# Optimization experiments

Hardware: AMD Instinct MI355X
Metric: run time of the kernel (lower is better)

Reference implementation:

```python
import jax, jax.numpy as jnp
import numpy as np

B, C, H, W = 32, 256, 32, 32   # batch, channels (inplanes==planes), spatial
E = 8                          # num_experts
EPS = 1e-5                     # BatchNorm eps


def setup_inputs() -> dict:
    key = jax.random.key(0)
    ks = jax.random.split(key, 6)
    s = 0.05
    return {
        "x": jax.random.normal(ks[0], (B, C, H, W), dtype=jnp.float32),
        # router: GAP -> Linear(C, E) -> sigmoid
        "router_w": jax.random.normal(ks[1], (E, C), dtype=jnp.float32) * s,
        "router_b": jnp.zeros((E,), dtype=jnp.float32),
        # expert kernel banks for the two CondConv2d layers (OIHW per expert)
        "w1": jax.random.normal(ks[2], (E, C, C, 3, 3), dtype=jnp.float32) * s,
        "w2": jax.random.normal(ks[3], (E, C, C, 3, 3), dtype=jnp.float32) * s,
        # BatchNorm (eval mode: running stats) params for bn1/bn2
        "g1": jnp.ones((C,), jnp.float32), "b1": jnp.zeros((C,), jnp.float32),
        "m1": jnp.zeros((C,), jnp.float32), "v1": jnp.ones((C,), jnp.float32),
        "g2": jnp.ones((C,), jnp.float32), "b2": jnp.zeros((C,), jnp.float32),
        "m2": jnp.zeros((C,), jnp.float32), "v2": jnp.ones((C,), jnp.float32),
    }


def _bn(x, g, b, m, v):
    # eval-mode BatchNorm over channel dim 1
    scale = (g * jax.lax.rsqrt(v + EPS))[None, :, None, None]
    shift = (b - m * g * jax.lax.rsqrt(v + EPS))[None, :, None, None]
    return x * scale + shift


def _cond_conv(x, w_bank, r):
    # x: [B,C,H,W]; w_bank: [E,O,I,3,3]; r: [B,E]
    # combine expert kernels per sample, then per-sample 3x3 conv (pad=1, stride=1)
    k = jnp.einsum('be,eoihw->boihw', r, w_bank)  # [B,O,I,3,3]

    def one(xb, kb):
        return jax.lax.conv_general_dilated(
            xb[None], kb, window_strides=(1, 1), padding=[(1, 1), (1, 1)],
            dimension_numbers=('NCHW', 'OIHW', 'NCHW'))[0]

    return jax.vmap(one)(x, k)  # [B,O,H,W]


def reference(x, router_w, router_b, w1, w2, g1, b1, m1, v1, g2, b2, m2, v2):
    # BasicRouter: global average pool -> linear -> sigmoid
    r = jax.nn.sigmoid(jnp.mean(x, axis=(2, 3)) @ router_w.T + router_b)  # [B,E]
    # drop_expert is identity in eval mode (training=False)
    out = jax.nn.relu(_bn(_cond_conv(x, w1, r), g1, b1, m1, v1))
    out = _bn(_cond_conv(out, w2, r), g2, b2, m2, v2)
    return jax.nn.relu(out + x)  # identity residual (stride=1, inplanes==planes)
```

## Files before the change

### kernel.cpp

```cpp
#include <hip/hip_runtime.h>

typedef unsigned short ushort_t;
typedef __attribute__((ext_vector_type(8))) __bf16 bf16x8;
typedef __attribute__((ext_vector_type(4))) float f32x4;
typedef __attribute__((ext_vector_type(4))) int i32x4;
typedef __attribute__((ext_vector_type(4))) unsigned short u16x4;

#define BN_EPS 1e-5f
#define EPAD 136

#define BAR()    __builtin_amdgcn_s_barrier()
#define VMCNT4() asm volatile("s_waitcnt vmcnt(4)" ::: "memory")
#define VMCNT0() asm volatile("s_waitcnt vmcnt(0)" ::: "memory")
#define LGKM0()  asm volatile("s_waitcnt lgkmcnt(0)" ::: "memory")

__device__ __forceinline__ ushort_t f2bf(float f) {
    union { float f; unsigned u; } v; v.f = f;
    unsigned r = v.u + 0x7FFFu + ((v.u >> 16) & 1u);
    return (ushort_t)(r >> 16);
}
__device__ __forceinline__ float bf2f(ushort_t h) {
    union { unsigned u; float f; } v; v.u = ((unsigned)h) << 16; return v.f;
}

__device__ __forceinline__ void async_cp16(const ushort_t* g, ushort_t* l) {
    __builtin_amdgcn_global_load_lds(
        (const __attribute__((address_space(1))) unsigned int*)g,
        (__attribute__((address_space(3))) unsigned int*)l, 16, 0, 0);
}

__global__ void transpose_gap_kernel(const float* __restrict__ x, ushort_t* __restrict__ xt,
                                     float* __restrict__ gapsum) {
    __shared__ float tile[32][33];
    int b = blockIdx.z, c0 = blockIdx.y * 32, p0 = blockIdx.x * 32;
    int tx = threadIdx.x & 31, ty = threadIdx.x >> 5;
    float ps[4];
    #pragma unroll
    for (int i = 0; i < 4; ++i) {
        int c = ty + i * 8;
        float v = x[((long)b * 256 + c0 + c) * 1024 + p0 + tx];
        tile[c][tx] = v;
        ps[i] = v;
    }
    #pragma unroll
    for (int off = 16; off; off >>= 1)
        #pragma unroll
        for (int i = 0; i < 4; ++i) ps[i] += __shfl_down(ps[i], off, 32);
    if (tx == 0)
        #pragma unroll
        for (int i = 0; i < 4; ++i) atomicAdd(&gapsum[b * 256 + c0 + ty + i * 8], ps[i]);
    __syncthreads();
    #pragma unroll
    for (int i = 0; i < 4; ++i) {
        int p = ty + i * 8;
        xt[((long)b * 1024 + p0 + p) * 256 + c0 + tx] = f2bf(tile[tx][p]);
    }
}

__global__ void router_linear_kernel(const float* __restrict__ gapsum, const float* __restrict__ rw,
                                     const float* __restrict__ rb, float* __restrict__ r) {
    int t = threadIdx.x, b = t >> 3, e = t & 7;
    float s = 0.f;
    for (int c = 0; c < 256; ++c) s += gapsum[b * 256 + c] * rw[e * 256 + c];
    r[t] = 1.f / (1.f + expf(-(s * (1.f / 1024.f) + rb[e])));
}

__global__ __launch_bounds__(256, 4) void combine_kernel(const float* __restrict__ w,
                                                         const float* __restrict__ r,
                                                         ushort_t* __restrict__ ko) {
    __shared__ float wl[9216];
    const int t = threadIdx.x;
    const int g0 = blockIdx.x * 128;
    const int b0 = blockIdx.y * 8;

    #pragma unroll
    for (int it = 0; it < 9; ++it) {
        int lin = it * 256 + t;
        int e = lin / 288, rem = lin - e * 288;
        f32x4 v = *(const f32x4*)(w + (long)e * 589824 + (long)g0 * 9 + rem * 4);
        *(f32x4*)(&wl[lin * 4]) = v;
    }
    __syncthreads();

    const int g = t & 127;
    const int half = t >> 7;
    float wv[8][9];
    #pragma unroll
    for (int e = 0; e < 8; ++e)
        #pragma unroll
        for (int p = 0; p < 9; ++p)
            wv[e][p] = wl[e * 1152 + g * 9 + p];

    #pragma unroll
    for (int j = 0; j < 4; ++j) {
        int b = b0 + half * 4 + j;
        float rv[8];
        #pragma unroll
        for (int e = 0; e < 8; ++e) rv[e] = r[b * 8 + e];
        #pragma unroll
        for (int p = 0; p < 9; ++p) {
            float s = 0.f;
            #pragma unroll
            for (int e = 0; e < 8; ++e) s += rv[e] * wv[e][p];
            ko[((long)(b * 9 + p)) * 65536 + g0 + g] = f2bf(s);
        }
    }
}

template <int MODE>
__global__ __launch_bounds__(256, 2) void gemm_conv(
    const ushort_t* __restrict__ xin,
    const ushort_t* __restrict__ kbank,
    void* __restrict__ outp,
    const float* __restrict__ gam, const float* __restrict__ bet,
    const float* __restrict__ mu, const float* __restrict__ var,
    const ushort_t* __restrict__ residt) {
    __shared__ ushort_t smem[29440];
    ushort_t* ldsB = smem;
    ushort_t* ldsA = smem + 13056;

    const int t = threadIdx.x;
    const int lane = t & 63;
    const int lane15 = lane & 15;
    const int quad = lane >> 4;
    const int wv = t >> 6;
    const int id = blockIdx.x;
    const int q  = id >> 3;
    const int mt = q & 1;
    const int nt = (q >> 1) & 7;
    const int b  = (id & 7) + ((q >> 4) << 3);
    const int h0 = nt * 4;
    const int p0 = nt * 128;
    const int mw0 = (wv >> 1) * 64;
    const int nw0 = (wv & 1) * 64;
    const int wbase = t & ~63;

    f32x4 acc[4][4];
    #pragma unroll
    for (int i = 0; i < 4; ++i)
        #pragma unroll
        for (int j = 0; j < 4; ++j) acc[i][j] = 0.f;

    if (t < 96) {
        int rix = t >> 3, j = t & 7;
        int pi = (rix >> 1) * 34 + (rix & 1) * 33;
        i32x4 z = 0;
        *(i32x4*)(&ldsB[(pi * 8 + j) * 8]) = z;
    }
    if (nt == 0) { i32x4 z = 0; *(i32x4*)(&ldsB[(8 + t) * 8]) = z; }
    if (nt == 7) { i32x4 z = 0; *(i32x4*)(&ldsB[((5 * 34 + 1) * 8 + t) * 8]) = z; }

    const long xbase = (long)b * 1024 * 256;
    const long kbase = (long)b * 9 * 65536;

    auto stageB = [&](int kc) {
        #pragma unroll
        for (int hh = 0; hh < 6; ++hh) {
            int hg = h0 + hh - 1;
            if (hg < 0 || hg >= 32) continue;
            int ww = t >> 3;
            int pi = hh * 34 + 1 + ww;
            int jd = (t & 7) ^ (pi & 7);
            async_cp16(xin + xbase + (long)(hg * 32 + ww) * 256 + kc * 64 + jd * 8,
                       ldsB + ((hh * 34 + 1) * 8 + wbase) * 8);
        }
    };
    auto stageA = [&](int kc, int pos, int buf) {
        const ushort_t* srcA = kbank + kbase + (long)pos * 65536 + (long)mt * 32768 + kc * 64;
        ushort_t* base = ldsA + buf * 8192;
        #pragma unroll
        for (int it = 0; it < 4; ++it) {
            int s = it * 256 + t;
            int row = s >> 3;
            int k8 = (s & 7) ^ (row & 7);
            async_cp16(srcA + (long)row * 256 + k8 * 8, base + (it * 256 + wbase) * 8);
        }
    };

    stageB(0);
    stageA(0, 0, 0);
    __syncthreads();

    int par = 0;
    for (int kc = 0; kc < 4; ++kc) {
        for (int pos = 0; pos < 9; ++pos) {
            const bool last = (kc == 3 && pos == 8);
            if (!last) {
                int nk = kc, np = pos + 1;
                if (np == 9) { np = 0; ++nk; }
                stageA(nk, np, par ^ 1);
                VMCNT4();
            } else {
                VMCNT0();
            }
            BAR();

            const int dh = pos / 3 - 1, dw = pos % 3 - 1;
            const ushort_t* ab = ldsA + par * 8192;
            bf16x8 af[2][4], bv[2][4];
            #pragma unroll
            for (int kb = 0; kb < 2; ++kb) {
                int jk = kb * 4 + quad;
                #pragma unroll
                for (int mf = 0; mf < 4; ++mf) {
                    int row = mw0 + mf * 16 + lane15;
                    af[kb][mf] = *(const bf16x8*)(ab + (row * 8 + (jk ^ (row & 7))) * 8);
                }
                #pragma unroll
                for (int nf = 0; nf < 4; ++nf) {
                    int n = nw0 + nf * 16 + lane15;
                    int pi = ((n >> 5) + 1 + dh) * 34 + (n & 31) + 1 + dw;
                    bv[kb][nf] = *(const bf16x8*)(&ldsB[(pi * 8 + (jk ^ (pi & 7))) * 8]);
                }
            }
            LGKM0();
            BAR();

            if (pos == 8 && kc < 3) stageB(kc + 1);

            __builtin_amdgcn_s_setprio(1);
            #pragma unroll
            for (int kb = 0; kb < 2; ++kb)
                #pragma unroll
                for (int mf = 0; mf < 4; ++mf)
                    #pragma unroll
                    for (int nf = 0; nf < 4; ++nf)
                        acc[mf][nf] = __builtin_amdgcn_mfma_f32_16x16x32_bf16(af[kb][mf], bv[kb][nf], acc[mf][nf], 0, 0, 0);
            __builtin_amdgcn_s_setprio(0);
            par ^= 1;
        }
    }

    u16x4 rres[4][4];
    if (MODE == 1) {
        #pragma unroll
        for (int mf = 0; mf < 4; ++mf)
            #pragma unroll
            for (int nf = 0; nf < 4; ++nf) {
                int p = p0 + nw0 + nf * 16 + lane15;
                int cb = mt * 128 + mw0 + mf * 16 + quad * 4;
                rres[mf][nf] = *(const u16x4*)(residt + ((long)b * 1024 + p) * 256 + cb);
            }
    }

    float sc[4][4], sh[4][4];
    #pragma unroll
    for (int mf = 0; mf < 4; ++mf)
        #pragma unroll
        for (int i = 0; i < 4; ++i) {
            int c = mt * 128 + mw0 + mf * 16 + quad * 4 + i;
            float s = gam[c] * rsqrtf(var[c] + BN_EPS);
            sc[mf][i] = s;
            sh[mf][i] = bet[c] - mu[c] * s;
        }

    if (MODE == 0) {
        __syncthreads();
        ushort_t* ldsE = smem;
        #pragma unroll
        for (int mf = 0; mf < 4; ++mf)
            #pragma unroll
            for (int nf = 0; nf < 4; ++nf) {
                int pl = nw0 + nf * 16 + lane15;
                int cb = mw0 + mf * 16 + quad * 4;
                u16x4 pk;
                #pragma unroll
                for (int i = 0; i < 4; ++i) {
                    float v = acc[mf][nf][i] * sc[mf][i] + sh[mf][i];
                    pk[i] = f2bf(fmaxf(v, 0.f));
                }
                *(u16x4*)(&ldsE[pl * EPAD + cb]) = pk;
            }
        __syncthreads();
        ushort_t* op = (ushort_t*)outp;
        #pragma unroll
        for (int it = 0; it < 8; ++it) {
            int s = t + it * 256;
            int row = s >> 4, l16 = s & 15;
            i32x4 v = *(i32x4*)(&ldsE[row * EPAD + l16 * 8]);
            *(i32x4*)(op + ((long)b * 1024 + p0 + row) * 256 + mt * 128 + l16 * 8) = v;
        }
    } else {
        float* op = (float*)outp;
        #pragma unroll
        for (int mf = 0; mf < 4; ++mf)
            #pragma unroll
            for (int nf = 0; nf < 4; ++nf) {
                int p = p0 + nw0 + nf * 16 + lane15;
                #pragma unroll
                for (int i = 0; i < 4; ++i) {
                    int c = mt * 128 + mw0 + mf * 16 + quad * 4 + i;
                    float v = acc[mf][nf][i] * sc[mf][i] + sh[mf][i] + bf2f(rres[mf][nf][i]);
                    op[((long)b * 256 + c) * 1024 + p] = fmaxf(v, 0.f);
                }
            }
    }
}

extern "C" void kernel_launch(void* const* d_in, const int* in_sizes, int n_in,
                              void* d_out, int out_size, void* d_ws, size_t ws_size,
                              hipStream_t stream) {
    const float* x  = (const float*)d_in[0];
    const float* rw = (const float*)d_in[1];
    const float* rb = (const float*)d_in[2];
    const float* w1 = (const float*)d_in[3];
    const float* w2 = (const float*)d_in[4];
    const float* g1 = (const float*)d_in[5];
    const float* b1 = (const float*)d_in[6];
    const float* m1 = (const float*)d_in[7];
    const float* v1 = (const float*)d_in[8];
    const float* g2 = (const float*)d_in[9];
    const float* b2 = (const float*)d_in[10];
    const float* m2 = (const float*)d_in[11];
    const float* v2 = (const float*)d_in[12];

    const size_t GAP_OFF = 4096;
    const size_t XT_OFF  = 36864;
    const size_t O1_OFF  = XT_OFF + (size_t)16777216;
    const size_t KB_OFF  = O1_OFF + (size_t)16777216;
    const size_t NEED    = KB_OFF + (size_t)32 * 9 * 65536 * 2;
    if (ws_size < NEED) return;

    char* ws = (char*)d_ws;
    float* r       = (float*)ws;
    float* gapsum  = (float*)(ws + GAP_OFF);
    ushort_t* xt   = (ushort_t*)(ws + XT_OFF);
    ushort_t* o1   = (ushort_t*)(ws + O1_OFF);
    ushort_t* kbuf = (ushort_t*)(ws + KB_OFF);

    hipMemsetAsync(gapsum, 0, 32768, stream);
    transpose_gap_kernel<<<dim3(32, 8, 32), 256, 0, stream>>>(x, xt, gapsum);
    router_linear_kernel<<<1, 256, 0, stream>>>(gapsum, rw, rb, r);
    combine_kernel<<<dim3(512, 4), 256, 0, stream>>>(w1, r, kbuf);
    gemm_conv<0><<<512, 256, 0, stream>>>(xt, kbuf, (void*)o1, g1, b1, m1, v1, nullptr);
    combine_kernel<<<dim3(512, 4), 256, 0, stream>>>(w2, r, kbuf);
    gemm_conv<1><<<512, 256, 0, stream>>>(o1, kbuf, d_out, g2, b2, m2, v2, xt);
}
```

Measured before the change: 255.0 us.

## Load conv weight tiles straight to registers, drop LDS staging and per-iteration barriers

```diff
diff --git a/kernel.cpp b/kernel.cpp
--- a/kernel.cpp
+++ b/kernel.cpp
@@ -10,7 +10,7 @@
 #define EPAD 136
 
 #define BAR()    __builtin_amdgcn_s_barrier()
-#define VMCNT4() asm volatile("s_waitcnt vmcnt(4)" ::: "memory")
+#define VMCNT8() asm volatile("s_waitcnt vmcnt(8)" ::: "memory")
 #define VMCNT0() asm volatile("s_waitcnt vmcnt(0)" ::: "memory")
 #define LGKM0()  asm volatile("s_waitcnt lgkmcnt(0)" ::: "memory")
 
@@ -115,9 +115,9 @@
     const float* __restrict__ gam, const float* __restrict__ bet,
     const float* __restrict__ mu, const float* __restrict__ var,
     const ushort_t* __restrict__ residt) {
-    __shared__ ushort_t smem[29440];
+    constexpr int SMEMN = (MODE == 0) ? 17408 : 13056;
+    __shared__ ushort_t smem[SMEMN];
     ushort_t* ldsB = smem;
-    ushort_t* ldsA = smem + 13056;
 
     const int t = threadIdx.x;
     const int lane = t & 63;
@@ -165,47 +165,42 @@
                        ldsB + ((hh * 34 + 1) * 8 + wbase) * 8);
         }
     };
-    auto stageA = [&](int kc, int pos, int buf) {
-        const ushort_t* srcA = kbank + kbase + (long)pos * 65536 + (long)mt * 32768 + kc * 64;
-        ushort_t* base = ldsA + buf * 8192;
-        #pragma unroll
-        for (int it = 0; it < 4; ++it) {
-            int s = it * 256 + t;
-            int row = s >> 3;
-            int k8 = (s & 7) ^ (row & 7);
-            async_cp16(srcA + (long)row * 256 + k8 * 8, base + (it * 256 + wbase) * 8);
-        }
+    const int arow = mt * 128 + mw0 + lane15;
+    auto issueA = [&](int kc, int pos, bf16x8* dst) {
+        const ushort_t* srcA = kbank + kbase + (long)pos * 65536 + kc * 64 + quad * 8;
+        #pragma unroll
+        for (int kb = 0; kb < 2; ++kb)
+            #pragma unroll
+            for (int mf = 0; mf < 4; ++mf)
+                dst[kb * 4 + mf] = *(const bf16x8*)(srcA + (long)(arow + mf * 16) * 256 + kb * 32);
     };
 
+    bf16x8 abuf[2][8];
     stageB(0);
-    stageA(0, 0, 0);
+    issueA(0, 0, abuf[0]);
     __syncthreads();
 
-    int par = 0;
+    #pragma unroll
     for (int kc = 0; kc < 4; ++kc) {
+        #pragma unroll
         for (int pos = 0; pos < 9; ++pos) {
-            const bool last = (kc == 3 && pos == 8);
+            const int it = kc * 9 + pos;
+            const bool last = (it == 35);
             if (!last) {
                 int nk = kc, np = pos + 1;
                 if (np == 9) { np = 0; ++nk; }
-                stageA(nk, np, par ^ 1);
-                VMCNT4();
+                issueA(nk, np, abuf[(it + 1) & 1]);
+                VMCNT8();
             } else {
                 VMCNT0();
             }
-            BAR();
+            if (pos == 0) BAR();
 
             const int dh = pos / 3 - 1, dw = pos % 3 - 1;
-            const ushort_t* ab = ldsA + par * 8192;
-            bf16x8 af[2][4], bv[2][4];
+            bf16x8 bv[2][4];
             #pragma unroll
             for (int kb = 0; kb < 2; ++kb) {
                 int jk = kb * 4 + quad;
-                #pragma unroll
-                for (int mf = 0; mf < 4; ++mf) {
-                    int row = mw0 + mf * 16 + lane15;
-                    af[kb][mf] = *(const bf16x8*)(ab + (row * 8 + (jk ^ (row & 7))) * 8);
-                }
                 #pragma unroll
                 for (int nf = 0; nf < 4; ++nf) {
                     int n = nw0 + nf * 16 + lane15;
@@ -213,11 +208,13 @@
                     bv[kb][nf] = *(const bf16x8*)(&ldsB[(pi * 8 + (jk ^ (pi & 7))) * 8]);
                 }
             }
-            LGKM0();
-            BAR();
-
-            if (pos == 8 && kc < 3) stageB(kc + 1);
-
+            if (pos == 8 && kc < 3) {
+                LGKM0();
+                BAR();
+                stageB(kc + 1);
+            }
+
+            const bf16x8* af = abuf[it & 1];
             __builtin_amdgcn_s_setprio(1);
             #pragma unroll
             for (int kb = 0; kb < 2; ++kb)
@@ -225,9 +222,8 @@
                 for (int mf = 0; mf < 4; ++mf)
                     #pragma unroll
                     for (int nf = 0; nf < 4; ++nf)
-                        acc[mf][nf] = __builtin_amdgcn_mfma_f32_16x16x32_bf16(af[kb][mf], bv[kb][nf], acc[mf][nf], 0, 0, 0);
+                        acc[mf][nf] = __builtin_amdgcn_mfma_f32_16x16x32_bf16(af[kb * 4 + mf], bv[kb][nf], acc[mf][nf], 0, 0, 0);
             __builtin_amdgcn_s_setprio(0);
-            par ^= 1;
         }
     }
 
```

Measured after the change: 323.1 us. 1.27x slower.

## Load conv weight fragments directly from global into registers for first conv

Applied to the files above, without the earlier changes.

```diff
diff --git a/kernel.cpp b/kernel.cpp
--- a/kernel.cpp
+++ b/kernel.cpp
@@ -11,6 +11,7 @@
 
 #define BAR()    __builtin_amdgcn_s_barrier()
 #define VMCNT4() asm volatile("s_waitcnt vmcnt(4)" ::: "memory")
+#define VMCNT8() asm volatile("s_waitcnt vmcnt(8)" ::: "memory")
 #define VMCNT0() asm volatile("s_waitcnt vmcnt(0)" ::: "memory")
 #define LGKM0()  asm volatile("s_waitcnt lgkmcnt(0)" ::: "memory")
 
@@ -107,7 +108,7 @@
     }
 }
 
-template <int MODE>
+template <int MODE, int APATH>
 __global__ __launch_bounds__(256, 2) void gemm_conv(
     const ushort_t* __restrict__ xin,
     const ushort_t* __restrict__ kbank,
@@ -115,9 +116,9 @@
     const float* __restrict__ gam, const float* __restrict__ bet,
     const float* __restrict__ mu, const float* __restrict__ var,
     const ushort_t* __restrict__ residt) {
-    __shared__ ushort_t smem[29440];
+    constexpr int SMEMN = (APATH == 0) ? 29440 : ((MODE == 0) ? 17408 : 13056);
+    __shared__ ushort_t smem[SMEMN];
     ushort_t* ldsB = smem;
-    ushort_t* ldsA = smem + 13056;
 
     const int t = threadIdx.x;
     const int lane = t & 63;
@@ -165,70 +166,132 @@
                        ldsB + ((hh * 34 + 1) * 8 + wbase) * 8);
         }
     };
-    auto stageA = [&](int kc, int pos, int buf) {
-        const ushort_t* srcA = kbank + kbase + (long)pos * 65536 + (long)mt * 32768 + kc * 64;
-        ushort_t* base = ldsA + buf * 8192;
-        #pragma unroll
-        for (int it = 0; it < 4; ++it) {
-            int s = it * 256 + t;
-            int row = s >> 3;
-            int k8 = (s & 7) ^ (row & 7);
-            async_cp16(srcA + (long)row * 256 + k8 * 8, base + (it * 256 + wbase) * 8);
-        }
-    };
-
-    stageB(0);
-    stageA(0, 0, 0);
-    __syncthreads();
-
-    int par = 0;
-    for (int kc = 0; kc < 4; ++kc) {
-        for (int pos = 0; pos < 9; ++pos) {
-            const bool last = (kc == 3 && pos == 8);
-            if (!last) {
-                int nk = kc, np = pos + 1;
-                if (np == 9) { np = 0; ++nk; }
-                stageA(nk, np, par ^ 1);
-                VMCNT4();
-            } else {
-                VMCNT0();
+
+    if constexpr (APATH == 0) {
+        ushort_t* ldsA = smem + 13056;
+        auto stageA = [&](int kc, int pos, int buf) {
+            const ushort_t* srcA = kbank + kbase + (long)pos * 65536 + (long)mt * 32768 + kc * 64;
+            ushort_t* base = ldsA + buf * 8192;
+            #pragma unroll
+            for (int it = 0; it < 4; ++it) {
+                int s = it * 256 + t;
+                int row = s >> 3;
+                int k8 = (s & 7) ^ (row & 7);
+                async_cp16(srcA + (long)row * 256 + k8 * 8, base + (it * 256 + wbase) * 8);
             }
-            BAR();
-
-            const int dh = pos / 3 - 1, dw = pos % 3 - 1;
-            const ushort_t* ab = ldsA + par * 8192;
-            bf16x8 af[2][4], bv[2][4];
-            #pragma unroll
-            for (int kb = 0; kb < 2; ++kb) {
-                int jk = kb * 4 + quad;
+        };
+
+        stageB(0);
+        stageA(0, 0, 0);
+        __syncthreads();
+
+        int par = 0;
+        for (int kc = 0; kc < 4; ++kc) {
+            for (int pos = 0; pos < 9; ++pos) {
+                const bool last = (kc == 3 && pos == 8);
+                if (!last) {
+                    int nk = kc, np = pos + 1;
+                    if (np == 9) { np = 0; ++nk; }
+                    stageA(nk, np, par ^ 1);
+                    VMCNT4();
+                } else {
+                    VMCNT0();
+                }
+                BAR();
+
+                const int dh = pos / 3 - 1, dw = pos % 3 - 1;
+                const ushort_t* ab = ldsA + par * 8192;
+                bf16x8 af[2][4], bfr[2][4];
                 #pragma unroll
-                for (int mf = 0; mf < 4; ++mf) {
-                    int row = mw0 + mf * 16 + lane15;
-                    af[kb][mf] = *(const bf16x8*)(ab + (row * 8 + (jk ^ (row & 7))) * 8);
+                for (int kb = 0; kb < 2; ++kb) {
+                    int jk = kb * 4 + quad;
+                    #pragma unroll
+                    for (int mf = 0; mf < 4; ++mf) {
+                        int row = mw0 + mf * 16 + lane15;
+                        af[kb][mf] = *(const bf16x8*)(ab + (row * 8 + (jk ^ (row & 7))) * 8);
+                    }
+                    #pragma unroll
+                    for (int nf = 0; nf < 4; ++nf) {
+                        int n = nw0 + nf * 16 + lane15;
+                        int pi = ((n >> 5) + 1 + dh) * 34 + (n & 31) + 1 + dw;
+                        bfr[kb][nf] = *(const bf16x8*)(&ldsB[(pi * 8 + (jk ^ (pi & 7))) * 8]);
+                    }
                 }
+                LGKM0();
+                BAR();
+
+                if (pos == 8 && kc < 3) stageB(kc + 1);
+
+                __builtin_amdgcn_s_setprio(1);
                 #pragma unroll
-                for (int nf = 0; nf < 4; ++nf) {
-                    int n = nw0 + nf * 16 + lane15;
-                    int pi = ((n >> 5) + 1 + dh) * 34 + (n & 31) + 1 + dw;
-                    bv[kb][nf] = *(const bf16x8*)(&ldsB[(pi * 8 + (jk ^ (pi & 7))) * 8]);
-                }
+                for (int kb = 0; kb < 2; ++kb)
+                    #pragma unroll
+                    for (int mf = 0; mf < 4; ++mf)
+                        #pragma unroll
+                        for (int nf = 0; nf < 4; ++nf)
+                            acc[mf][nf] = __builtin_amdgcn_mfma_f32_16x16x32_bf16(af[kb][mf], bfr[kb][nf], acc[mf][nf], 0, 0, 0);
+                __builtin_amdgcn_s_setprio(0);
+                par ^= 1;
             }
-            LGKM0();
-            BAR();
-
-            if (pos == 8 && kc < 3) stageB(kc + 1);
-
-            __builtin_amdgcn_s_setprio(1);
-            #pragma unroll
-            for (int kb = 0; kb < 2; ++kb)
-                #pragma unroll
-                for (int mf = 0; mf < 4; ++mf)
-                    #pragma unroll
-                    for (int nf = 0; nf < 4; ++nf)
-                        acc[mf][nf] = __builtin_amdgcn_mfma_f32_16x16x32_bf16(af[kb][mf], bv[kb][nf], acc[mf][nf], 0, 0, 0);
-            __builtin_amdgcn_s_setprio(0);
-            par ^= 1;
-        }
+        }
+    } else {
+        const int arow = mt * 128 + mw0 + lane15;
+        const long abase = kbase + (long)arow * 256 + quad * 8;
+        bf16x8 abufA[8], abufB[8];
+
+#define ISSUEA(nk, np, dst) {                                                     \
+        const ushort_t* sA = kbank + abase + ((np) * 65536 + (nk) * 64);          \
+        _Pragma("unroll")                                                         \
+        for (int kb = 0; kb < 2; ++kb)                                            \
+            _Pragma("unroll")                                                     \
+            for (int mf = 0; mf < 4; ++mf)                                        \
+                dst[kb * 4 + mf] = *(const bf16x8*)(sA + (long)(mf * 16) * 256 + kb * 32); }
+
+#define STEP(cur, nxt) {                                                          \
+        const int itx = kc * 9 + pos;                                             \
+        if (itx != 35) {                                                          \
+            int np = pos + 1, nk = kc;                                            \
+            if (np == 9) { np = 0; ++nk; }                                        \
+            ISSUEA(nk, np, nxt);                                                  \
+            VMCNT8();                                                             \
+        } else { VMCNT0(); }                                                      \
+        if (pos == 0) BAR();                                                      \
+        const int dh = pos / 3 - 1, dw = pos % 3 - 1;                             \
+        bf16x8 bv[2][4];                                                          \
+        _Pragma("unroll")                                                         \
+        for (int kb = 0; kb < 2; ++kb) {                                          \
+            int jk = kb * 4 + quad;                                               \
+            _Pragma("unroll")                                                     \
+            for (int nf = 0; nf < 4; ++nf) {                                      \
+                int n = nw0 + nf * 16 + lane15;                                   \
+                int pi = ((n >> 5) + 1 + dh) * 34 + (n & 31) + 1 + dw;            \
+                bv[kb][nf] = *(const bf16x8*)(&ldsB[(pi * 8 + (jk ^ (pi & 7))) * 8]); \
+            } }                                                                   \
+        if (pos == 8 && kc < 3) { LGKM0(); BAR(); stageB(kc + 1); }               \
+        __builtin_amdgcn_s_setprio(1);                                            \
+        _Pragma("unroll")                                                         \
+        for (int kb = 0; kb < 2; ++kb)                                            \
+            _Pragma("unroll")                                                     \
+            for (int mf = 0; mf < 4; ++mf)                                        \
+                _Pragma("unroll")                                                 \
+                for (int nf = 0; nf < 4; ++nf)                                    \
+                    acc[mf][nf] = __builtin_amdgcn_mfma_f32_16x16x32_bf16(cur[kb * 4 + mf], bv[kb][nf], acc[mf][nf], 0, 0, 0); \
+        __builtin_amdgcn_s_setprio(0);                                            \
+        ++pos; if (pos == 9) { pos = 0; ++kc; }                                   \
+}
+
+        stageB(0);
+        ISSUEA(0, 0, abufA);
+        __syncthreads();
+
+        int kc = 0, pos = 0;
+        #pragma unroll 1
+        for (int d = 0; d < 18; ++d) {
+            STEP(abufA, abufB)
+            STEP(abufB, abufA)
+        }
+#undef STEP
+#undef ISSUEA
     }
 
     u16x4 rres[4][4];
@@ -332,7 +395,7 @@
     transpose_gap_kernel<<<dim3(32, 8, 32), 256, 0, stream>>>(x, xt, gapsum);
     router_linear_kernel<<<1, 256, 0, stream>>>(gapsum, rw, rb, r);
     combine_kernel<<<dim3(512, 4), 256, 0, stream>>>(w1, r, kbuf);
-    gemm_conv<0><<<512, 256, 0, stream>>>(xt, kbuf, (void*)o1, g1, b1, m1, v1, nullptr);
+    gemm_conv<0, 1><<<512, 256, 0, stream>>>(xt, kbuf, (void*)o1, g1, b1, m1, v1, nullptr);
     combine_kernel<<<dim3(512, 4), 256, 0, stream>>>(w2, r, kbuf);
-    gemm_conv<1><<<512, 256, 0, stream>>>(o1, kbuf, d_out, g2, b2, m2, v2, xt);
-}
+    gemm_conv<1, 0><<<512, 256, 0, stream>>>(o1, kbuf, d_out, g2, b2, m2, v2, xt);
+}
```

Result: slower. 287.6 us (+12.8%).
